# Performance work log

Hardware: AMD Instinct MI355X
Metric: run time of the kernel (lower is better)

The kernel has to match this reference:

```python
import jax, jax.numpy as jnp
import numpy as np
from jax import lax

INPUT, HIDDEN, LAYERS = 256, 512, 2
B, T = 128, 512


def setup_inputs() -> dict:
    key = jax.random.key(0)
    ks = jax.random.split(key, 8)
    s_in = 1.0 / np.sqrt(HIDDEN)
    x = jax.random.normal(ks[0], (B, T, INPUT), dtype=jnp.float32)
    # PyTorch LSTM layout: W_ih [4H, in], W_hh [4H, H], gate order (i, f, g, o).
    w_ih0 = jax.random.uniform(ks[1], (4 * HIDDEN, INPUT), jnp.float32, -s_in, s_in)
    w_hh0 = jax.random.uniform(ks[2], (4 * HIDDEN, HIDDEN), jnp.float32, -s_in, s_in)
    b0 = jax.random.uniform(ks[3], (4 * HIDDEN,), jnp.float32, -s_in, s_in)  # b_ih + b_hh combined
    w_ih1 = jax.random.uniform(ks[4], (4 * HIDDEN, HIDDEN), jnp.float32, -s_in, s_in)
    w_hh1 = jax.random.uniform(ks[5], (4 * HIDDEN, HIDDEN), jnp.float32, -s_in, s_in)
    b1 = jax.random.uniform(ks[6], (4 * HIDDEN,), jnp.float32, -s_in, s_in)
    # fc: xavier_uniform weight, bias init to constant 30 per init_weights()
    lim = np.sqrt(6.0 / (HIDDEN + 1))
    fc_w = jax.random.uniform(ks[7], (1, HIDDEN), jnp.float32, -lim, lim)
    fc_b = jnp.full((1,), 30.0, dtype=jnp.float32)
    return {"x": x, "w_ih0": w_ih0, "w_hh0": w_hh0, "b0": b0,
            "w_ih1": w_ih1, "w_hh1": w_hh1, "b1": b1,
            "fc_w": fc_w, "fc_b": fc_b}


def _lstm_layer(x, w_ih, w_hh, b):
    # x: [B, T, D] -> outputs [B, T, H], final hidden [B, H]
    Bb, Tt = x.shape[0], x.shape[1]
    H = w_hh.shape[1]
    # Precompute input projection for all timesteps (big GEMM).
    xg = jnp.einsum('btd,gd->btg', x, w_ih) + b  # [B, T, 4H]
    h0 = jnp.zeros((Bb, H), dtype=x.dtype)
    c0 = jnp.zeros((Bb, H), dtype=x.dtype)

    def step(carry, xt):
        h, c = carry
        g = xt + h @ w_hh.T  # [B, 4H]
        i, f, gg, o = jnp.split(g, 4, axis=-1)
        c = jax.nn.sigmoid(f) * c + jax.nn.sigmoid(i) * jnp.tanh(gg)
        h = jax.nn.sigmoid(o) * jnp.tanh(c)
        return (h, c), h

    (hT, cT), ys = lax.scan(step, (h0, c0), xg.transpose(1, 0, 2))
    return ys.transpose(1, 0, 2), hT


def reference(x, w_ih0, w_hh0, b0, w_ih1, w_hh1, b1, fc_w, fc_b):
    y0, h0 = _lstm_layer(x, w_ih0, w_hh0, b0)
    y1, h1 = _lstm_layer(y0, w_ih1, w_hh1, b1)
    hn = jnp.concatenate([h0, h1], axis=0)  # hn.view(-1, H): [L*B, H]
    return hn @ fc_w.T + fc_b  # [L*B, 1]
```

## Files before the change

### kernel.cpp

```cpp
#include <hip/hip_runtime.h>
#include <stdint.h>


using s16x8 = __attribute__((ext_vector_type(8))) short;
using f32x4 = __attribute__((ext_vector_type(4))) float;
typedef unsigned long long ull;

#define WSB1_OFF 1572864
#define HB0_OFF  3670016
#define HB1_OFF  3801088
#define TAGS_BYTE_OFF 7864320

__device__ __forceinline__ float bf2f(unsigned short u) {
    unsigned v = ((unsigned)u) << 16;
    return __builtin_bit_cast(float, v);
}
__device__ __forceinline__ unsigned short f2bf(float f) {
    unsigned x = __builtin_bit_cast(unsigned, f);
    x += 0x7FFFu + ((x >> 16) & 1u);
    return (unsigned short)(x >> 16);
}
__device__ __forceinline__ float sigm(float x) { return 1.f / (1.f + __expf(-x)); }
__device__ __forceinline__ float tanhc(float x) {
    x = fminf(15.f, fmaxf(-15.f, x));
    float e = __expf(-2.f * x);
    return (1.f - e) / (1.f + e);
}
__device__ __forceinline__ unsigned tagld(const unsigned* p) {
    return __hip_atomic_load(p, __ATOMIC_RELAXED, __HIP_MEMORY_SCOPE_SYSTEM);
}

__device__ __forceinline__ void store_frag(unsigned short* dst, int n, int kc, int KT,
                                           const float* src) {
    s16x8 v;
#pragma unroll
    for (int e = 0; e < 8; ++e) v[e] = (short)f2bf(src[e]);
    int gate = n >> 9, hid = n & 511;
    int rt = hid >> 5;
    int w  = (hid >> 3) & 3;
    int t  = gate >> 1;
    int lo = (gate & 1) * 8 + (hid & 7);
    int tileIdx = w * 2 + t;
    int kt = kc >> 2, q = kc & 3;
    int lane = q * 16 + lo;
    size_t off = ((((size_t)rt * 8 + tileIdx) * KT + kt) * 64 + lane) * 8;
    *(s16x8*)(dst + off) = v;
}

__global__ void k_prep(const float* __restrict__ wih0, const float* __restrict__ whh0,
                       const float* __restrict__ wih1, const float* __restrict__ whh1,
                       unsigned short* __restrict__ wsB0, unsigned short* __restrict__ wsB1,
                       unsigned short* __restrict__ hb0, unsigned short* __restrict__ hb1,
                       unsigned* __restrict__ tags) {
    int idx = blockIdx.x * 256 + threadIdx.x;
    if (idx < 196608) {
        int n = idx / 96, kc = idx - n * 96;
        int k = kc * 8;
        const float* src = (k < 256) ? (wih0 + (size_t)n * 256 + k)
                                     : (whh0 + (size_t)n * 512 + (k - 256));
        store_frag(wsB0, n, kc, 24, src);
    } else if (idx < 458752) {
        int j = idx - 196608;
        int n = j >> 7, kc = j & 127;
        int k = kc * 8;
        const float* src = (k < 512) ? (wih1 + (size_t)n * 512 + k)
                                     : (whh1 + (size_t)n * 512 + (k - 512));
        store_frag(wsB1, n, kc, 32, src);
    } else {
        int z = idx - 458752;
        if (z < 8192) {
            ull* p = (ull*)(hb0 + 65536 + (size_t)z * 8);
            p[0] = 0ull; p[1] = 0ull;
        } else if (z < 16384) {
            ull* p = (ull*)(hb1 + (size_t)(z - 8192) * 8);
            p[0] = 0ull; p[1] = 0ull;
        } else if (z < 16640) {
            tags[(size_t)(z - 16384) * 32] = 0u;
        }
    }
}

template <int LAYER, int KT>
__device__ __forceinline__ void run_layer(const float* __restrict__ x,
                                          const unsigned short* __restrict__ wsB,
                                          unsigned short* hsrc0,
                                          unsigned short* hself,
                                          unsigned* tags,
                                          unsigned* mytag,
                                          float bv0, float bv1,
                                          int g, int rt, int w, int lane, int tid,
                                          char* At) {
    constexpr int PITCH = (LAYER == 0) ? 1600 : 2112;
    constexpr int KTX   = 8;
    constexpr int KTY   = 16;
    const int lm = lane & 15, lq = lane >> 4;

    s16x8 bfr0[KT], bfr1[KT];
    {
        const unsigned short* base = wsB + (((size_t)rt * 8 + 2 * w) * KT) * 512;
#pragma unroll
        for (int kt = 0; kt < KT; ++kt) {
            bfr0[kt] = *(const s16x8*)(base + ((size_t)kt * 64 + lane) * 8);
            bfr1[kt] = *(const s16x8*)(base + (((size_t)KT + kt) * 64 + lane) * 8);
        }
    }

    float cst[4] = {0.f, 0.f, 0.f, 0.f};

    f32x4 xa[2], xb[2];
    int xrow[2], xch[2];
    if (LAYER == 0) {
#pragma unroll
        for (int i = 0; i < 2; ++i) {
            int task = tid + i * 256;
            xrow[i] = task >> 5; xch[i] = task & 31;
            const float* src = x + ((size_t)(g * 16 + xrow[i]) * 512) * 256 + xch[i] * 8;
            xa[i] = *(const f32x4*)(src);
            xb[i] = *(const f32x4*)(src + 4);
        }
    }

#pragma unroll 1
    for (int s = 0; s <= 512; ++s) {
        const bool active = LAYER ? (s >= 1) : (s < 512);
        const int pr = (s + 1) & 1;
        const int pw = s & 1;

        if (active) {
            f32x4 acc0 = {0.f, 0.f, 0.f, 0.f}, acc1 = {0.f, 0.f, 0.f, 0.f};
            const char* ap = At + lm * PITCH + lq * 16;

            if (LAYER == 0) {
#pragma unroll
                for (int i = 0; i < 2; ++i) {
                    s16x8 v;
#pragma unroll
                    for (int e = 0; e < 4; ++e) { v[e] = (short)f2bf(xa[i][e]); v[4 + e] = (short)f2bf(xb[i][e]); }
                    *(s16x8*)(At + xrow[i] * PITCH + xch[i] * 16) = v;
                }
                if (s + 1 < 512) {
#pragma unroll
                    for (int i = 0; i < 2; ++i) {
                        const float* src = x + ((size_t)(g * 16 + xrow[i]) * 512 + (s + 1)) * 256 + xch[i] * 8;
                        xa[i] = *(const f32x4*)(src);
                        xb[i] = *(const f32x4*)(src + 4);
                    }
                }
                __syncthreads();

#pragma unroll
                for (int kt = 0; kt < KTX; ++kt) {
                    s16x8 a = *(const s16x8*)(ap + kt * 64);
                    acc0 = __builtin_amdgcn_mfma_f32_16x16x32_bf16(a, bfr0[kt], acc0, 0, 0, 0);
                    acc1 = __builtin_amdgcn_mfma_f32_16x16x32_bf16(a, bfr1[kt], acc1, 0, 0, 0);
                }

                if (tid < 16) {
                    unsigned* tp = tags + (size_t)tid * 32;
                    while (tagld(tp) < (unsigned)s) __builtin_amdgcn_s_sleep(1);
                }
                __syncthreads();

#pragma unroll
                for (int i = 0; i < 4; ++i) {
                    int task = tid + i * 256;
                    int row = task >> 6, c8 = task & 63;
                    const ull* sp = (const ull*)(hsrc0 + (size_t)(pr * 128 + g * 16 + row) * 512 + c8 * 8);
                    ull v0 = __hip_atomic_load(sp,     __ATOMIC_RELAXED, __HIP_MEMORY_SCOPE_SYSTEM);
                    ull v1 = __hip_atomic_load(sp + 1, __ATOMIC_RELAXED, __HIP_MEMORY_SCOPE_SYSTEM);
                    ull* d = (ull*)(At + row * PITCH + 512 + c8 * 16);
                    d[0] = v0; d[1] = v1;
                }
                __syncthreads();

#pragma unroll
                for (int kt = KTX; kt < KT; ++kt) {
                    s16x8 a = *(const s16x8*)(ap + kt * 64);
                    acc0 = __builtin_amdgcn_mfma_f32_16x16x32_bf16(a, bfr0[kt], acc0, 0, 0, 0);
                    acc1 = __builtin_amdgcn_mfma_f32_16x16x32_bf16(a, bfr1[kt], acc1, 0, 0, 0);
                }
            } else {
                if (tid < 16) {
                    unsigned* tp = tags + (size_t)(16 + tid) * 32;
                    while (tagld(tp) < (unsigned)s) __builtin_amdgcn_s_sleep(1);
                }
                __syncthreads();

#pragma unroll
                for (int i = 0; i < 4; ++i) {
                    int task = tid + i * 256;
                    int row = task >> 6, c8 = task & 63;
                    const ull* sp = (const ull*)(hself + (size_t)(pr * 128 + g * 16 + row) * 512 + c8 * 8);
                    ull v0 = __hip_atomic_load(sp,     __ATOMIC_RELAXED, __HIP_MEMORY_SCOPE_SYSTEM);
                    ull v1 = __hip_atomic_load(sp + 1, __ATOMIC_RELAXED, __HIP_MEMORY_SCOPE_SYSTEM);
                    ull* d = (ull*)(At + row * PITCH + 1024 + c8 * 16);
                    d[0] = v0; d[1] = v1;
                }
                __syncthreads();

#pragma unroll
                for (int kt = KTY; kt < KT; ++kt) {
                    s16x8 a = *(const s16x8*)(ap + kt * 64);
                    acc0 = __builtin_amdgcn_mfma_f32_16x16x32_bf16(a, bfr0[kt], acc0, 0, 0, 0);
                    acc1 = __builtin_amdgcn_mfma_f32_16x16x32_bf16(a, bfr1[kt], acc1, 0, 0, 0);
                }

                if (tid < 16) {
                    unsigned* tp = tags + (size_t)tid * 32;
                    while (tagld(tp) < (unsigned)s) __builtin_amdgcn_s_sleep(1);
                }
                __syncthreads();

#pragma unroll
                for (int i = 0; i < 4; ++i) {
                    int task = tid + i * 256;
                    int row = task >> 6, c8 = task & 63;
                    const ull* sp = (const ull*)(hsrc0 + (size_t)(pr * 128 + g * 16 + row) * 512 + c8 * 8);
                    ull v0 = __hip_atomic_load(sp,     __ATOMIC_RELAXED, __HIP_MEMORY_SCOPE_SYSTEM);
                    ull v1 = __hip_atomic_load(sp + 1, __ATOMIC_RELAXED, __HIP_MEMORY_SCOPE_SYSTEM);
                    ull* d = (ull*)(At + row * PITCH + c8 * 16);
                    d[0] = v0; d[1] = v1;
                }
                __syncthreads();

#pragma unroll
                for (int kt = 0; kt < KTY; ++kt) {
                    s16x8 a = *(const s16x8*)(ap + kt * 64);
                    acc0 = __builtin_amdgcn_mfma_f32_16x16x32_bf16(a, bfr0[kt], acc0, 0, 0, 0);
                    acc1 = __builtin_amdgcn_mfma_f32_16x16x32_bf16(a, bfr1[kt], acc1, 0, 0, 0);
                }
            }

            const bool hi = (lm & 8) != 0;
            float hv[4];
#pragma unroll
            for (int r = 0; r < 4; ++r) {
                float a0 = acc0[r] + bv0;
                float a1 = acc1[r] + bv1;
                float a0x = __shfl_xor(a0, 8, 16);
                float a1x = __shfl_xor(a1, 8, 16);
                float iv = hi ? a0x : a0;
                float fv = hi ? a0  : a0x;
                float gv = hi ? a1x : a1;
                float ov = hi ? a1  : a1x;
                float cn = sigm(fv) * cst[r] + sigm(iv) * tanhc(gv);
                cst[r] = cn;
                hv[r] = sigm(ov) * tanhc(cn);
            }

            if (LAYER == 0) {
                if (tid < 16) {
                    unsigned* tp = tags + (size_t)(16 + tid) * 32;
                    while (tagld(tp) < (unsigned)s) __builtin_amdgcn_s_sleep(1);
                }
                __syncthreads();
            }

            ull packed = 0;
#pragma unroll
            for (int r = 0; r < 4; ++r)
                packed |= ((ull)f2bf(hv[r])) << (16 * r);
            ull outp = 0;
            const int rp = (lm >> 1) & 3;
#pragma unroll
            for (int e = 0; e < 4; ++e) {
                ull got = __shfl(packed, (lm & 1) * 4 + e, 16);
                ull val = (got >> (16 * rp)) & 0xFFFFull;
                outp |= val << (16 * e);
            }
            if (lm < 8) {
                int brow = lq * 4 + (lm >> 1);
                size_t off = (size_t)(pw * 128 + g * 16 + brow) * 512
                           + rt * 32 + w * 8 + (lm & 1) * 4;
                __hip_atomic_store((ull*)(hself + off), outp,
                                   __ATOMIC_RELAXED, __HIP_MEMORY_SCOPE_SYSTEM);
            }
        }

        __syncthreads();
        if (tid == 0)
            __hip_atomic_store(mytag, (unsigned)(s + 1),
                               __ATOMIC_RELAXED, __HIP_MEMORY_SCOPE_SYSTEM);
    }
}

__launch_bounds__(256, 1)
__global__ void k_lstm(const float* __restrict__ x,
                       const float* __restrict__ b0,
                       const float* __restrict__ b1,
                       const unsigned short* __restrict__ wsB0,
                       const unsigned short* __restrict__ wsB1,
                       unsigned short* hb0, unsigned short* hb1,
                       unsigned* tags) {
    __shared__ __align__(16) char Atile[16 * 2112];

    const int tid = threadIdx.x;
    const int g = blockIdx.x & 7, sub = blockIdx.x >> 3;
    const int layer = sub >> 4, rt = sub & 15;
    const int w = tid >> 6, lane = tid & 63;
    const int lm = lane & 15;

    unsigned* gtags = tags + (size_t)g * 32 * 32;
    unsigned* mytag = gtags + (size_t)(layer * 16 + rt) * 32;

    const float* bias = layer ? b1 : b0;
    const int jsub = rt * 32 + w * 8 + (lm & 7);
    const int G0 = (lm & 8) ? 1 : 0;
    const float bv0 = bias[G0 * 512 + jsub];
    const float bv1 = bias[(G0 + 2) * 512 + jsub];

    if (layer == 0)
        run_layer<0, 24>(x, wsB0, hb0, hb0, gtags, mytag, bv0, bv1,
                         g, rt, w, lane, tid, Atile);
    else
        run_layer<1, 32>(x, wsB1, hb0, hb1, gtags, mytag, bv0, bv1,
                         g, rt, w, lane, tid, Atile);
}

__global__ void k_fc(const unsigned short* __restrict__ hb0,
                     const unsigned short* __restrict__ hb1,
                     const float* __restrict__ fcw, const float* __restrict__ fcb,
                     float* __restrict__ out) {
    int i = blockIdx.x, lane = threadIdx.x;
    const unsigned short* hrow = (i < 128) ? (hb0 + (size_t)(128 + i) * 512)
                                           : (hb1 + (size_t)(i - 128) * 512);
    float ssum = 0.f;
    int j0 = lane * 8;
#pragma unroll
    for (int e = 0; e < 8; ++e) ssum += bf2f(hrow[j0 + e]) * fcw[j0 + e];
#pragma unroll
    for (int off2 = 32; off2 > 0; off2 >>= 1) ssum += __shfl_down(ssum, off2);
    if (lane == 0) out[i] = ssum + fcb[0];
}

extern "C" void kernel_launch(void* const* d_in, const int* in_sizes, int n_in,
                              void* d_out, int out_size, void* d_ws, size_t ws_size,
                              hipStream_t stream) {
    const float* x    = (const float*)d_in[0];
    const float* wih0 = (const float*)d_in[1];
    const float* whh0 = (const float*)d_in[2];
    const float* b0   = (const float*)d_in[3];
    const float* wih1 = (const float*)d_in[4];
    const float* whh1 = (const float*)d_in[5];
    const float* b1   = (const float*)d_in[6];
    const float* fcw  = (const float*)d_in[7];
    const float* fcb  = (const float*)d_in[8];

    unsigned short* wsB0 = (unsigned short*)d_ws;
    unsigned short* wsB1 = wsB0 + WSB1_OFF;
    unsigned short* hb0  = wsB0 + HB0_OFF;
    unsigned short* hb1  = wsB0 + HB1_OFF;
    unsigned* tags = (unsigned*)((char*)d_ws + TAGS_BYTE_OFF);
    float* out = (float*)d_out;

    k_prep<<<dim3(1857), dim3(256), 0, stream>>>(wih0, whh0, wih1, whh1,
                                                 wsB0, wsB1, hb0, hb1, tags);

    k_lstm<<<dim3(256), dim3(256), 0, stream>>>(x, b0, b1, wsB0, wsB1, hb0, hb1, tags);

    k_fc<<<dim3(256), dim3(64), 0, stream>>>(hb0, hb1, fcw, fcb, out);
}
```

Measured before the change: 2.656 ms.

## Triple-buffer layer-0 hidden state and pack tags to loosen inter-layer sync

Adds a three-slot ring buffer for layer-0 hidden states, used when the workspace is large enough. With it, layer 0 no longer waits for layer 1 to consume the previous slot before writing and needs only one polling barrier per step. The tags are packed contiguously instead of padded to 128 bytes. Polling now uses inline-asm double-issued loads that bypass the cache, and the h loads are hoisted ahead of the x-part MFMAs to overlap latency. The risks are tag false sharing, since all tags of a group now share cache lines, and dependence on the workspace size.

```diff
diff --git a/kernel.cpp b/kernel.cpp
--- a/kernel.cpp
+++ b/kernel.cpp
@@ -8,8 +8,7 @@
 
 #define WSB1_OFF 1572864
 #define HB0_OFF  3670016
-#define HB1_OFF  3801088
-#define TAGS_BYTE_OFF 7864320
+#define SLOT_W   65536
 
 __device__ __forceinline__ float bf2f(unsigned short u) {
     unsigned v = ((unsigned)u) << 16;
@@ -26,8 +25,27 @@
     float e = __expf(-2.f * x);
     return (1.f - e) / (1.f + e);
 }
-__device__ __forceinline__ unsigned tagld(const unsigned* p) {
-    return __hip_atomic_load(p, __ATOMIC_RELAXED, __HIP_MEMORY_SCOPE_SYSTEM);
+
+__device__ __forceinline__ void poll_ge2(const unsigned* tp, unsigned thr) {
+    unsigned a, b;
+    asm volatile("global_load_dword %0, %2, off sc0 sc1\n\t"
+                 "global_load_dword %1, %2, off sc0 sc1"
+                 : "=&v"(a), "=&v"(b) : "v"(tp) : "memory");
+    for (;;) {
+        asm volatile("s_waitcnt vmcnt(1)" : "+v"(a) : : "memory");
+        __builtin_amdgcn_sched_barrier(0);
+        if (a >= thr) break;
+        asm volatile("global_load_dword %0, %1, off sc0 sc1"
+                     : "=&v"(a) : "v"(tp) : "memory");
+        asm volatile("s_waitcnt vmcnt(1)" : "+v"(b) : : "memory");
+        __builtin_amdgcn_sched_barrier(0);
+        if (b >= thr) break;
+        asm volatile("global_load_dword %0, %1, off sc0 sc1"
+                     : "=&v"(b) : "v"(tp) : "memory");
+        __builtin_amdgcn_s_sleep(1);
+    }
+    asm volatile("s_waitcnt vmcnt(0)" ::: "memory");
+    __builtin_amdgcn_sched_barrier(0);
 }
 
 __device__ __forceinline__ void store_frag(unsigned short* dst, int n, int kc, int KT,
@@ -51,7 +69,7 @@
                        const float* __restrict__ wih1, const float* __restrict__ whh1,
                        unsigned short* __restrict__ wsB0, unsigned short* __restrict__ wsB1,
                        unsigned short* __restrict__ hb0, unsigned short* __restrict__ hb1,
-                       unsigned* __restrict__ tags) {
+                       unsigned* __restrict__ tags, int d3) {
     int idx = blockIdx.x * 256 + threadIdx.x;
     if (idx < 196608) {
         int n = idx / 96, kc = idx - n * 96;
@@ -69,23 +87,23 @@
     } else {
         int z = idx - 458752;
         if (z < 8192) {
-            ull* p = (ull*)(hb0 + 65536 + (size_t)z * 8);
+            ull* p = (ull*)(hb0 + (d3 ? 2 * SLOT_W : SLOT_W) + (size_t)z * 8);
             p[0] = 0ull; p[1] = 0ull;
         } else if (z < 16384) {
             ull* p = (ull*)(hb1 + (size_t)(z - 8192) * 8);
             p[0] = 0ull; p[1] = 0ull;
         } else if (z < 16640) {
-            tags[(size_t)(z - 16384) * 32] = 0u;
-        }
-    }
-}
-
-template <int LAYER, int KT>
+            tags[z - 16384] = 0u;
+        }
+    }
+}
+
+template <int LAYER, int KT, bool D3>
 __device__ __forceinline__ void run_layer(const float* __restrict__ x,
                                           const unsigned short* __restrict__ wsB,
                                           unsigned short* hsrc0,
                                           unsigned short* hself,
-                                          unsigned* tags,
+                                          unsigned* gt,
                                           unsigned* mytag,
                                           float bv0, float bv1,
                                           int g, int rt, int w, int lane, int tid,
@@ -120,11 +138,15 @@
         }
     }
 
+    int sw3 = 0, sr3 = 2;
+
 #pragma unroll 1
     for (int s = 0; s <= 512; ++s) {
         const bool active = LAYER ? (s >= 1) : (s < 512);
-        const int pr = (s + 1) & 1;
-        const int pw = s & 1;
+        const int rH = D3 ? sr3 : ((s + 1) & 1);
+        const int wH = D3 ? sw3 : (s & 1);
+        const int pr2 = (s + 1) & 1;
+        const int pw2 = s & 1;
 
         if (active) {
             f32x4 acc0 = {0.f, 0.f, 0.f, 0.f}, acc1 = {0.f, 0.f, 0.f, 0.f};
@@ -146,30 +168,38 @@
                         xb[i] = *(const f32x4*)(src + 4);
                     }
                 }
-                __syncthreads();
-
+
+                if (D3) {
+                    if (tid < 32) {
+                        unsigned thr = (tid < 16) ? (unsigned)s
+                                                  : (unsigned)(s > 0 ? s - 1 : 0);
+                        poll_ge2(gt + tid, thr);
+                    }
+                } else {
+                    if (tid < 16) poll_ge2(gt + tid, (unsigned)s);
+                }
+                __syncthreads();
+
+                ull hva[4], hvb[4];
+                int hrw[4], hc8[4];
+#pragma unroll
+                for (int i = 0; i < 4; ++i) {
+                    int task = tid + i * 256;
+                    hrw[i] = task >> 6; hc8[i] = task & 63;
+                    const ull* sp = (const ull*)(hsrc0 + (size_t)(rH * 128 + g * 16 + hrw[i]) * 512 + hc8[i] * 8);
+                    hva[i] = __hip_atomic_load(sp,     __ATOMIC_RELAXED, __HIP_MEMORY_SCOPE_SYSTEM);
+                    hvb[i] = __hip_atomic_load(sp + 1, __ATOMIC_RELAXED, __HIP_MEMORY_SCOPE_SYSTEM);
+                }
 #pragma unroll
                 for (int kt = 0; kt < KTX; ++kt) {
                     s16x8 a = *(const s16x8*)(ap + kt * 64);
                     acc0 = __builtin_amdgcn_mfma_f32_16x16x32_bf16(a, bfr0[kt], acc0, 0, 0, 0);
                     acc1 = __builtin_amdgcn_mfma_f32_16x16x32_bf16(a, bfr1[kt], acc1, 0, 0, 0);
                 }
-
-                if (tid < 16) {
-                    unsigned* tp = tags + (size_t)tid * 32;
-                    while (tagld(tp) < (unsigned)s) __builtin_amdgcn_s_sleep(1);
-                }
-                __syncthreads();
-
 #pragma unroll
                 for (int i = 0; i < 4; ++i) {
-                    int task = tid + i * 256;
-                    int row = task >> 6, c8 = task & 63;
-                    const ull* sp = (const ull*)(hsrc0 + (size_t)(pr * 128 + g * 16 + row) * 512 + c8 * 8);
-                    ull v0 = __hip_atomic_load(sp,     __ATOMIC_RELAXED, __HIP_MEMORY_SCOPE_SYSTEM);
-                    ull v1 = __hip_atomic_load(sp + 1, __ATOMIC_RELAXED, __HIP_MEMORY_SCOPE_SYSTEM);
-                    ull* d = (ull*)(At + row * PITCH + 512 + c8 * 16);
-                    d[0] = v0; d[1] = v1;
+                    ull* d = (ull*)(At + hrw[i] * PITCH + 512 + hc8[i] * 16);
+                    d[0] = hva[i]; d[1] = hvb[i];
                 }
                 __syncthreads();
 
@@ -180,17 +210,14 @@
                     acc1 = __builtin_amdgcn_mfma_f32_16x16x32_bf16(a, bfr1[kt], acc1, 0, 0, 0);
                 }
             } else {
-                if (tid < 16) {
-                    unsigned* tp = tags + (size_t)(16 + tid) * 32;
-                    while (tagld(tp) < (unsigned)s) __builtin_amdgcn_s_sleep(1);
-                }
+                if (tid < 16) poll_ge2(gt + 16 + tid, (unsigned)s);
                 __syncthreads();
 
 #pragma unroll
                 for (int i = 0; i < 4; ++i) {
                     int task = tid + i * 256;
                     int row = task >> 6, c8 = task & 63;
-                    const ull* sp = (const ull*)(hself + (size_t)(pr * 128 + g * 16 + row) * 512 + c8 * 8);
+                    const ull* sp = (const ull*)(hself + (size_t)(pr2 * 128 + g * 16 + row) * 512 + c8 * 8);
                     ull v0 = __hip_atomic_load(sp,     __ATOMIC_RELAXED, __HIP_MEMORY_SCOPE_SYSTEM);
                     ull v1 = __hip_atomic_load(sp + 1, __ATOMIC_RELAXED, __HIP_MEMORY_SCOPE_SYSTEM);
                     ull* d = (ull*)(At + row * PITCH + 1024 + c8 * 16);
@@ -205,17 +232,14 @@
                     acc1 = __builtin_amdgcn_mfma_f32_16x16x32_bf16(a, bfr1[kt], acc1, 0, 0, 0);
                 }
 
-                if (tid < 16) {
-                    unsigned* tp = tags + (size_t)tid * 32;
-                    while (tagld(tp) < (unsigned)s) __builtin_amdgcn_s_sleep(1);
-                }
+                if (tid < 16) poll_ge2(gt + tid, (unsigned)s);
                 __syncthreads();
 
 #pragma unroll
                 for (int i = 0; i < 4; ++i) {
                     int task = tid + i * 256;
                     int row = task >> 6, c8 = task & 63;
-                    const ull* sp = (const ull*)(hsrc0 + (size_t)(pr * 128 + g * 16 + row) * 512 + c8 * 8);
+                    const ull* sp = (const ull*)(hsrc0 + (size_t)(rH * 128 + g * 16 + row) * 512 + c8 * 8);
                     ull v0 = __hip_atomic_load(sp,     __ATOMIC_RELAXED, __HIP_MEMORY_SCOPE_SYSTEM);
                     ull v1 = __hip_atomic_load(sp + 1, __ATOMIC_RELAXED, __HIP_MEMORY_SCOPE_SYSTEM);
                     ull* d = (ull*)(At + row * PITCH + c8 * 16);
@@ -248,11 +272,8 @@
                 hv[r] = sigm(ov) * tanhc(cn);
             }
 
-            if (LAYER == 0) {
-                if (tid < 16) {
-                    unsigned* tp = tags + (size_t)(16 + tid) * 32;
-                    while (tagld(tp) < (unsigned)s) __builtin_amdgcn_s_sleep(1);
-                }
+            if (LAYER == 0 && !D3) {
+                if (tid < 16) poll_ge2(gt + 16 + tid, (unsigned)s);
                 __syncthreads();
             }
 
@@ -270,7 +291,8 @@
             }
             if (lm < 8) {
                 int brow = lq * 4 + (lm >> 1);
-                size_t off = (size_t)(pw * 128 + g * 16 + brow) * 512
+                int slot = (LAYER == 0) ? wH : pw2;
+                size_t off = (size_t)(slot * 128 + g * 16 + brow) * 512
                            + rt * 32 + w * 8 + (lm & 1) * 4;
                 __hip_atomic_store((ull*)(hself + off), outp,
                                    __ATOMIC_RELAXED, __HIP_MEMORY_SCOPE_SYSTEM);
@@ -278,9 +300,14 @@
         }
 
         __syncthreads();
-        if (tid == 0)
+        if (tid == 255)
             __hip_atomic_store(mytag, (unsigned)(s + 1),
                                __ATOMIC_RELAXED, __HIP_MEMORY_SCOPE_SYSTEM);
+
+        if (D3) {
+            sw3 = (sw3 == 2) ? 0 : sw3 + 1;
+            sr3 = (sr3 == 2) ? 0 : sr3 + 1;
+        }
     }
 }
 
@@ -291,7 +318,7 @@
                        const unsigned short* __restrict__ wsB0,
                        const unsigned short* __restrict__ wsB1,
                        unsigned short* hb0, unsigned short* hb1,
-                       unsigned* tags) {
+                       unsigned* tags, int d3) {
     __shared__ __align__(16) char Atile[16 * 2112];
 
     const int tid = threadIdx.x;
@@ -300,8 +327,8 @@
     const int w = tid >> 6, lane = tid & 63;
     const int lm = lane & 15;
 
-    unsigned* gtags = tags + (size_t)g * 32 * 32;
-    unsigned* mytag = gtags + (size_t)(layer * 16 + rt) * 32;
+    unsigned* gt = tags + (size_t)g * 32;
+    unsigned* mytag = gt + layer * 16 + rt;
 
     const float* bias = layer ? b1 : b0;
     const int jsub = rt * 32 + w * 8 + (lm & 7);
@@ -309,20 +336,25 @@
     const float bv0 = bias[G0 * 512 + jsub];
     const float bv1 = bias[(G0 + 2) * 512 + jsub];
 
-    if (layer == 0)
-        run_layer<0, 24>(x, wsB0, hb0, hb0, gtags, mytag, bv0, bv1,
-                         g, rt, w, lane, tid, Atile);
-    else
-        run_layer<1, 32>(x, wsB1, hb0, hb1, gtags, mytag, bv0, bv1,
-                         g, rt, w, lane, tid, Atile);
-}
-
-__global__ void k_fc(const unsigned short* __restrict__ hb0,
+    if (layer == 0) {
+        if (d3) run_layer<0, 24, true >(x, wsB0, hb0, hb0, gt, mytag, bv0, bv1,
+                                        g, rt, w, lane, tid, Atile);
+        else    run_layer<0, 24, false>(x, wsB0, hb0, hb0, gt, mytag, bv0, bv1,
+                                        g, rt, w, lane, tid, Atile);
+    } else {
+        if (d3) run_layer<1, 32, true >(x, wsB1, hb0, hb1, gt, mytag, bv0, bv1,
+                                        g, rt, w, lane, tid, Atile);
+        else    run_layer<1, 32, false>(x, wsB1, hb0, hb1, gt, mytag, bv0, bv1,
+                                        g, rt, w, lane, tid, Atile);
+    }
+}
+
+__global__ void k_fc(const unsigned short* __restrict__ hb0fin,
                      const unsigned short* __restrict__ hb1,
                      const float* __restrict__ fcw, const float* __restrict__ fcb,
                      float* __restrict__ out) {
     int i = blockIdx.x, lane = threadIdx.x;
-    const unsigned short* hrow = (i < 128) ? (hb0 + (size_t)(128 + i) * 512)
+    const unsigned short* hrow = (i < 128) ? (hb0fin + (size_t)i * 512)
                                            : (hb1 + (size_t)(i - 128) * 512);
     float ssum = 0.f;
     int j0 = lane * 8;
@@ -346,17 +378,21 @@
     const float* fcw  = (const float*)d_in[7];
     const float* fcb  = (const float*)d_in[8];
 
+    const int d3 = (ws_size >= (size_t)7996416) ? 1 : 0;
+
     unsigned short* wsB0 = (unsigned short*)d_ws;
     unsigned short* wsB1 = wsB0 + WSB1_OFF;
     unsigned short* hb0  = wsB0 + HB0_OFF;
-    unsigned short* hb1  = wsB0 + HB1_OFF;
-    unsigned* tags = (unsigned*)((char*)d_ws + TAGS_BYTE_OFF);
+    unsigned short* hb1  = hb0 + (d3 ? 3 : 2) * SLOT_W;
+    unsigned* tags = (unsigned*)((char*)d_ws + (d3 ? 7995392 : 7864320));
+    unsigned short* hb0fin = hb0 + (d3 ? 2 : 1) * SLOT_W;
     float* out = (float*)d_out;
 
     k_prep<<<dim3(1857), dim3(256), 0, stream>>>(wih0, whh0, wih1, whh1,
-                                                 wsB0, wsB1, hb0, hb1, tags);
-
-    k_lstm<<<dim3(256), dim3(256), 0, stream>>>(x, b0, b1, wsB0, wsB1, hb0, hb1, tags);
-
-    k_fc<<<dim3(256), dim3(64), 0, stream>>>(hb0, hb1, fcw, fcb, out);
-}
+                                                 wsB0, wsB1, hb0, hb1, tags, d3);
+
+    k_lstm<<<dim3(256), dim3(256), 0, stream>>>(x, b0, b1, wsB0, wsB1, hb0, hb1,
+                                                tags, d3);
+
+    k_fc<<<dim3(256), dim3(64), 0, stream>>>(hb0fin, hb1, fcw, fcb, out);
+}
```

Result: slower. 3.649 ms (+37.4%).
